# Kernel optimization log

Hardware: AMD Instinct MI355X
Metric: run time of the kernel (lower is better)

Reference implementation:

```python
import jax, jax.numpy as jnp
import numpy as np
from jax import lax

MARGIN = 0.2
NMAX = 1


def setup_inputs() -> dict:
    key = jax.random.key(0)
    k1, k2 = jax.random.split(key)
    N, D = 8192, 512
    imgs = jax.random.normal(k1, (N, D), dtype=jnp.float32)
    caps = jax.random.normal(k2, (N, D), dtype=jnp.float32)
    return {"imgs": imgs, "caps": caps}


def reference(imgs, caps):
    # scores[i, j] = <img_i, cap_j>  -> [N, N]
    scores = jnp.matmul(imgs, caps.T)
    diag = jnp.diagonal(scores)  # [N]
    s = scores - 2.0 * jnp.diag(diag)
    # top-nmax over columns (axis 0): hardest negative captions per caption slot
    max_c = lax.top_k(s.T, NMAX)[0].T  # [NMAX, N]
    # top-nmax over rows (axis 1): hardest negative images per image slot
    max_i = lax.top_k(s, NMAX)[0]      # [N, NMAX]
    neg_cap = jnp.sum(jnp.maximum(max_c + (MARGIN - diag)[None, :], 0.0))
    neg_img = jnp.sum(jnp.maximum(max_i + (MARGIN - diag)[:, None], 0.0))
    return neg_cap + neg_img
```

## Files before the change

kernel.cpp:

```cpp
#include <hip/hip_runtime.h>

#define N_ROWS 8192
#define DIM    512

typedef __attribute__((ext_vector_type(4))) float frag_cd;
typedef __attribute__((ext_vector_type(2))) long long v2ll;

__device__ __forceinline__ unsigned f2fp8(float x) {
    float a = fabsf(x);
    unsigned s = (__float_as_uint(x) >> 31) << 7;
    if (a < 0.015625f) return s;
    a = fminf(a, 448.f);
    unsigned u = __float_as_uint(a);
    u += 0x7FFFFu + ((u >> 20) & 1u);
    unsigned exp = (u >> 23) - 120u;
    unsigned mant = (u >> 20) & 7u;
    return s | (exp << 3) | mant;
}
__device__ __forceinline__ unsigned pack4fp8(float4 v) {
    return f2fp8(v.x) | (f2fp8(v.y) << 8) | (f2fp8(v.z) << 16) | (f2fp8(v.w) << 24);
}
__device__ __forceinline__ unsigned enc_f32(float f) {
    unsigned u = __float_as_uint(f);
    return (u & 0x80000000u) ? ~u : (u | 0x80000000u);
}
__device__ __forceinline__ float dec_f32(unsigned k) {
    return __uint_as_float((k & 0x80000000u) ? (k & 0x7FFFFFFFu) : ~k);
}


__global__ __launch_bounds__(256) void k_prep(const float* __restrict__ imgs,
                                              const float* __restrict__ caps,
                                              unsigned char* __restrict__ fimgs,
                                              unsigned char* __restrict__ fcaps,
                                              float* __restrict__ diag,
                                              unsigned* __restrict__ rowmax,
                                              unsigned* __restrict__ colmax,
                                              float* __restrict__ out) {
    const int cr = blockIdx.x;
    const int t  = threadIdx.x;
    const int w = t >> 6, l = t & 63;
    const int kp = l >> 3, cg = l & 3, par = (l >> 2) & 1;
    if (cr == 0 && t == 0) out[0] = 0.f;
    const size_t ubase = (size_t)cr * 8192 + kp * 1024 + cg * 256 + par * 8;
    float ps[4];
    #pragma unroll
    for (int i = 0; i < 4; ++i) {
        const int row = w + 4 * i;
        const float* ar = imgs + ((size_t)cr * 16 + row) * DIM + l * 8;
        const float* br = caps + ((size_t)cr * 16 + row) * DIM + l * 8;
        float4 a0 = *(const float4*)ar, a1 = *(const float4*)(ar + 4);
        float4 b0 = *(const float4*)br, b1 = *(const float4*)(br + 4);
        uint2 oa, ob;
        oa.x = pack4fp8(a0); oa.y = pack4fp8(a1);
        ob.x = pack4fp8(b0); ob.y = pack4fp8(b1);
        *(uint2*)(fimgs + ubase + row * 16) = oa;
        *(uint2*)(fcaps + ubase + row * 16) = ob;
        ps[i] = a0.x * b0.x + a0.y * b0.y + a0.z * b0.z + a0.w * b0.w
              + a1.x * b1.x + a1.y * b1.y + a1.z * b1.z + a1.w * b1.w;
    }
    #pragma unroll
    for (int i = 0; i < 4; ++i) {
        float s = ps[i];
        #pragma unroll
        for (int m = 1; m < 64; m <<= 1) s += __shfl_xor(s, m, 64);
        if (l == 0) {
            const int r = cr * 16 + w + 4 * i;
            diag[r] = s; rowmax[r] = 0u; colmax[r] = 0u;
        }
    }
}

__global__ __launch_bounds__(256, 6) void k_gemm(const unsigned char* __restrict__ A,
                                                 const unsigned char* __restrict__ B,
                                                 unsigned* __restrict__ rowmax,
                                                 unsigned* __restrict__ colmax) {
    __shared__ unsigned char sA[2][4096];
    __shared__ unsigned char sB[2][8192];
    const int tid = threadIdx.x;
    const int w = tid >> 6, lane = tid & 63;
    const int f = (int)blockIdx.x;
    const int jb = (f & 7) * 8 + ((f >> 3) & 7);
    const int ib = f >> 6;
    const int j0 = jb << 7, i0 = ib << 6;
    const int q = lane >> 4, l15 = lane & 15;
    const int wr = (w & 1) << 5, wc = (w >> 1) << 6;

    const unsigned char* Ab = A + (size_t)(i0 >> 4) * 8192 + lane * 16;
    const unsigned char* Bb = B + (size_t)(j0 >> 4) * 8192 + lane * 16;

    frag_cd acc[2][4] = {};

    auto stage = [&](int bi, int kp) {
        __builtin_amdgcn_global_load_lds(
            (const __attribute__((address_space(1))) unsigned int*)(Ab + (size_t)w * 8192 + kp * 1024),
            (__attribute__((address_space(3))) unsigned int*)(&sA[bi][(w << 10) + (lane << 4)]), 16, 0, 0);
        #pragma unroll
        for (int j = 0; j < 2; ++j) {
            const int s = 2 * w + j;
            __builtin_amdgcn_global_load_lds(
                (const __attribute__((address_space(1))) unsigned int*)(Bb + (size_t)s * 8192 + kp * 1024),
                (__attribute__((address_space(3))) unsigned int*)(&sB[bi][(s << 10) + (lane << 4)]), 16, 0, 0);
        }
    };

    stage(0, 0);
    __syncthreads();

    const int u16 = ((q << 4) + l15) << 4;

    #pragma unroll
    for (int kp = 0; kp < 8; ++kp) {
        const int cur = kp & 1, nxt = cur ^ 1;
        if (kp < 7) stage(nxt, kp + 1);

        v2ll af[2], bfr[4];
        #pragma unroll
        for (int r = 0; r < 2; ++r)
            af[r] = *(const v2ll*)(&sA[cur][((((w & 1) << 1) + r) << 10) + u16]);
        #pragma unroll
        for (int c = 0; c < 4; ++c)
            bfr[c] = *(const v2ll*)(&sB[cur][((((w >> 1) << 2) + c) << 10) + u16]);
        #pragma unroll
        for (int r = 0; r < 2; ++r)
            #pragma unroll
            for (int c = 0; c < 4; ++c)
                acc[r][c] = __builtin_amdgcn_mfma_f32_16x16x32_fp8_fp8(af[r][0], bfr[c][0], acc[r][c], 0, 0, 0);
        #pragma unroll
        for (int r = 0; r < 2; ++r)
            #pragma unroll
            for (int c = 0; c < 4; ++c)
                acc[r][c] = __builtin_amdgcn_mfma_f32_16x16x32_fp8_fp8(af[r][1], bfr[c][1], acc[r][c], 0, 0, 0);

        if (kp < 7) __syncthreads();
    }

    const bool dblk = ((i0 >> 7) == jb);
    #pragma unroll
    for (int r = 0; r < 2; ++r)
        #pragma unroll
        for (int c = 0; c < 4; ++c)
            #pragma unroll
            for (int g = 0; g < 4; ++g) {
                float fv = acc[r][c][g];
                const int gi = wr + (r << 4) + (q << 2) + g;
                const int gj = wc + (c << 4) + l15;
                if (dblk && (i0 + gi) == (j0 + gj)) fv = -fv;
                acc[r][c][g] = fv;
            }

    #pragma unroll
    for (int r = 0; r < 2; ++r)
        #pragma unroll
        for (int g = 0; g < 4; ++g) {
            float m = fmaxf(fmaxf(acc[r][0][g], acc[r][1][g]),
                            fmaxf(acc[r][2][g], acc[r][3][g]));
            m = fmaxf(m, __shfl_xor(m, 1, 64));
            m = fmaxf(m, __shfl_xor(m, 2, 64));
            m = fmaxf(m, __shfl_xor(m, 4, 64));
            m = fmaxf(m, __shfl_xor(m, 8, 64));
            if (l15 == 0)
                atomicMax(&rowmax[i0 + wr + (r << 4) + (q << 2) + g], enc_f32(m));
        }
    #pragma unroll
    for (int c = 0; c < 4; ++c) {
        float m = acc[0][c][0];
        #pragma unroll
        for (int r = 0; r < 2; ++r)
            #pragma unroll
            for (int g = 0; g < 4; ++g) m = fmaxf(m, acc[r][c][g]);
        m = fmaxf(m, __shfl_xor(m, 16, 64));
        m = fmaxf(m, __shfl_xor(m, 32, 64));
        if (q == 0)
            atomicMax(&colmax[j0 + wc + (c << 4) + l15], enc_f32(m));
    }
}

__global__ __launch_bounds__(256) void k_final(const unsigned* __restrict__ rowmax,
                                               const unsigned* __restrict__ colmax,
                                               const float* __restrict__ diag,
                                               float* __restrict__ out) {
    const int idx = blockIdx.x * 256 + threadIdx.x;
    const float d = diag[idx];
    float s = fmaxf(dec_f32(rowmax[idx]) + 0.2f - d, 0.f)
            + fmaxf(dec_f32(colmax[idx]) + 0.2f - d, 0.f);
    #pragma unroll
    for (int m = 1; m < 64; m <<= 1) s += __shfl_xor(s, m, 64);
    __shared__ float red[4];
    if ((threadIdx.x & 63) == 0) red[threadIdx.x >> 6] = s;
    __syncthreads();
    if (threadIdx.x == 0)
        atomicAdd(out, red[0] + red[1] + red[2] + red[3]);
}

extern "C" void kernel_launch(void* const* d_in, const int* in_sizes, int n_in,
                              void* d_out, int out_size, void* d_ws, size_t ws_size,
                              hipStream_t stream) {
    const float* imgs = (const float*)d_in[0];
    const float* caps = (const float*)d_in[1];
    float* out = (float*)d_out;

    char* ws = (char*)d_ws;
    unsigned char* fimgs = (unsigned char*)ws;
    unsigned char* fcaps = (unsigned char*)(ws + 4194304);
    float*    diag   = (float*)   (ws + 8388608);
    unsigned* rowmax = (unsigned*)(ws + 8388608 + 32768);
    unsigned* colmax = (unsigned*)(ws + 8388608 + 65536);

    k_prep<<<N_ROWS / 16, 256, 0, stream>>>(imgs, caps, fimgs, fcaps,
                                            diag, rowmax, colmax, out);
    k_gemm<<<8192, 256, 0, stream>>>(fimgs, fcaps, rowmax, colmax);
    k_final<<<N_ROWS / 256, 256, 0, stream>>>(rowmax, colmax, diag, out);
}
```

Baseline: 158.8 us.

## Give each wave private LDS staging to drop block-wide barriers in GEMM

```diff
diff --git a/kernel.cpp b/kernel.cpp
--- a/kernel.cpp
+++ b/kernel.cpp
@@ -71,12 +71,11 @@
     }
 }
 
-__global__ __launch_bounds__(256, 6) void k_gemm(const unsigned char* __restrict__ A,
+__global__ __launch_bounds__(256, 3) void k_gemm(const unsigned char* __restrict__ A,
                                                  const unsigned char* __restrict__ B,
                                                  unsigned* __restrict__ rowmax,
                                                  unsigned* __restrict__ colmax) {
-    __shared__ unsigned char sA[2][4096];
-    __shared__ unsigned char sB[2][8192];
+    __shared__ unsigned char sMem[4][12288];
     const int tid = threadIdx.x;
     const int w = tid >> 6, lane = tid & 63;
     const int f = (int)blockIdx.x;
@@ -85,42 +84,46 @@
     const int j0 = jb << 7, i0 = ib << 6;
     const int q = lane >> 4, l15 = lane & 15;
     const int wr = (w & 1) << 5, wc = (w >> 1) << 6;
-
-    const unsigned char* Ab = A + (size_t)(i0 >> 4) * 8192 + lane * 16;
-    const unsigned char* Bb = B + (size_t)(j0 >> 4) * 8192 + lane * 16;
+    const int u16 = ((q << 4) + l15) << 4;
+
+    unsigned char* myA = &sMem[w][0];
+    unsigned char* myB = &sMem[w][4096];
+    const unsigned char* Aw = A + (size_t)((i0 >> 4) + ((w & 1) << 1)) * 8192 + lane * 16;
+    const unsigned char* Bw = B + (size_t)((j0 >> 4) + ((w >> 1) << 2)) * 8192 + lane * 16;
+
+    auto stage = [&](int bi, int kp) {
+        #pragma unroll
+        for (int r = 0; r < 2; ++r)
+            __builtin_amdgcn_global_load_lds(
+                (const __attribute__((address_space(1))) unsigned int*)(Aw + (size_t)r * 8192 + kp * 1024),
+                (__attribute__((address_space(3))) unsigned int*)(myA + bi * 2048 + r * 1024 + lane * 16), 16, 0, 0);
+        #pragma unroll
+        for (int c = 0; c < 4; ++c)
+            __builtin_amdgcn_global_load_lds(
+                (const __attribute__((address_space(1))) unsigned int*)(Bw + (size_t)c * 8192 + kp * 1024),
+                (__attribute__((address_space(3))) unsigned int*)(myB + bi * 4096 + c * 1024 + lane * 16), 16, 0, 0);
+    };
 
     frag_cd acc[2][4] = {};
-
-    auto stage = [&](int bi, int kp) {
-        __builtin_amdgcn_global_load_lds(
-            (const __attribute__((address_space(1))) unsigned int*)(Ab + (size_t)w * 8192 + kp * 1024),
-            (__attribute__((address_space(3))) unsigned int*)(&sA[bi][(w << 10) + (lane << 4)]), 16, 0, 0);
-        #pragma unroll
-        for (int j = 0; j < 2; ++j) {
-            const int s = 2 * w + j;
-            __builtin_amdgcn_global_load_lds(
-                (const __attribute__((address_space(1))) unsigned int*)(Bb + (size_t)s * 8192 + kp * 1024),
-                (__attribute__((address_space(3))) unsigned int*)(&sB[bi][(s << 10) + (lane << 4)]), 16, 0, 0);
-        }
-    };
-
     stage(0, 0);
-    __syncthreads();
-
-    const int u16 = ((q << 4) + l15) << 4;
 
     #pragma unroll
     for (int kp = 0; kp < 8; ++kp) {
         const int cur = kp & 1, nxt = cur ^ 1;
-        if (kp < 7) stage(nxt, kp + 1);
+        if (kp < 7) {
+            stage(nxt, kp + 1);
+            __builtin_amdgcn_s_waitcnt(0x0F76);
+        } else {
+            __builtin_amdgcn_s_waitcnt(0x0F70);
+        }
 
         v2ll af[2], bfr[4];
         #pragma unroll
         for (int r = 0; r < 2; ++r)
-            af[r] = *(const v2ll*)(&sA[cur][((((w & 1) << 1) + r) << 10) + u16]);
+            af[r] = *(const v2ll*)(myA + cur * 2048 + r * 1024 + u16);
         #pragma unroll
         for (int c = 0; c < 4; ++c)
-            bfr[c] = *(const v2ll*)(&sB[cur][((((w >> 1) << 2) + c) << 10) + u16]);
+            bfr[c] = *(const v2ll*)(myB + cur * 4096 + c * 1024 + u16);
         #pragma unroll
         for (int r = 0; r < 2; ++r)
             #pragma unroll
@@ -131,8 +134,6 @@
             #pragma unroll
             for (int c = 0; c < 4; ++c)
                 acc[r][c] = __builtin_amdgcn_mfma_f32_16x16x32_fp8_fp8(af[r][1], bfr[c][1], acc[r][c], 0, 0, 0);
-
-        if (kp < 7) __syncthreads();
     }
 
     const bool dblk = ((i0 >> 7) == jb);
```

Result: slower. 183.6 us (+15.6%).
